# Optimization experiments

Hardware: AMD Instinct MI355X
Metric: run time of the kernel (lower is better)

Reference implementation:

```python
import jax, jax.numpy as jnp
import numpy as np

S, B, H, N, D = 1024, 4, 1024, 16, 64  # seq, batch, d_model, heads, head_dim
P = 2 * S  # relative position length (klen + qlen, no memory)


def rel_shift(x, klen):
    # x: [q, p, b, n] -> shift so position j aligns relatively, keep klen cols
    q, p, b, n = x.shape
    x = jnp.reshape(x, (p, q, b, n))[1:]
    x = jnp.reshape(x, (q, p - 1, b, n))[:, :klen]
    return x


def setup_inputs():
    key = jax.random.key(0)
    ks = jax.random.split(key, 12)
    f32 = jnp.float32
    attention_input = jax.random.normal(ks[0], (S, B, H), f32)
    pos_emb = jax.random.normal(ks[1], (P, B, H), f32)
    seg_embed = jax.random.normal(ks[2], (2, N, D), f32) * 0.02
    # segment matrix: one-hot of whether tokens i,j are in different segments
    seg_ids = jax.random.randint(ks[3], (S, B), 0, 2)
    diff = (seg_ids[:, None, :] != seg_ids[None, :, :]).astype(jnp.int32)
    seg_mat = jax.nn.one_hot(diff, 2, dtype=f32)  # [S,S,B,2]
    r_w_bias = jax.random.normal(ks[4], (N, D), f32) * 0.02
    r_r_bias = jax.random.normal(ks[5], (N, D), f32) * 0.02
    r_s_bias = jax.random.normal(ks[6], (N, D), f32) * 0.02
    # causal mask: 1 where attention is disallowed (j > i)
    causal = jnp.triu(jnp.ones((S, S), f32), k=1)
    attn_mask = jnp.broadcast_to(causal[:, :, None, None], (S, S, B, 1))
    w = lambda k: jax.random.normal(k, (H, N, D), f32) * 0.02
    return {
        'attention_input': attention_input, 'pos_emb': pos_emb,
        'seg_embed': seg_embed, 'seg_mat': seg_mat,
        'r_w_bias': r_w_bias, 'r_r_bias': r_r_bias, 'r_s_bias': r_s_bias,
        'attn_mask': attn_mask,
        'Wq': w(ks[7]), 'Wk': w(ks[8]), 'Wv': w(ks[9]),
        'Wr': w(ks[10]), 'Wo': w(ks[11]),
    }


def reference(attention_input, pos_emb, seg_embed, seg_mat, r_w_bias,
              r_r_bias, r_s_bias, attn_mask, Wq, Wk, Wv, Wr, Wo):
    scale = 1.0 / (D ** 0.5)
    q = jnp.einsum('ibh,hnd->ibnd', attention_input, Wq)
    k = jnp.einsum('ibh,hnd->ibnd', attention_input, Wk)
    v = jnp.einsum('ibh,hnd->ibnd', attention_input, Wv)
    kr = jnp.einsum('ibh,hnd->ibnd', pos_emb, Wr)  # [P,B,N,D]
    # content-based score
    ac = jnp.einsum('ibnd,jbnd->ijbn', q + r_w_bias, k)
    # position-based score with relative shift
    bd = jnp.einsum('ibnd,jbnd->ijbn', q + r_r_bias, kr)
    bd = rel_shift(bd, ac.shape[1])
    # segment-based score
    ef = jnp.einsum('ibnd,snd->ibns', q + r_s_bias, seg_embed)
    ef = jnp.einsum('ijbs,ibns->ijbn', seg_mat, ef)
    attn_score = (ac + bd + ef) * scale - 1e30 * attn_mask
    attn_prob = jax.nn.softmax(attn_score, axis=1)
    attn_vec = jnp.einsum('ijbn,jbnd->ibnd', attn_prob, v)
    attn_out = jnp.einsum('ibnd,hnd->ibh', attn_vec, Wo)
    return attn_out
```

## Files before the change

kernel.cpp:

```cpp
#include <hip/hip_runtime.h>
#include <hip/hip_bf16.h>
#include <stdint.h>


typedef short short8 __attribute__((ext_vector_type(8)));
typedef __bf16 bf16x8 __attribute__((ext_vector_type(8)));
typedef float f32x4 __attribute__((ext_vector_type(4)));
typedef unsigned short u16;
typedef unsigned long long u64;

#define LOG2E 1.4426950408889634f

__device__ __forceinline__ u16 f2bf(float f) {
  union { float f; unsigned u; } v; v.f = f;
  unsigned u = v.u;
  u += 0x7fffu + ((u >> 16) & 1u);
  return (u16)(u >> 16);
}
__device__ __forceinline__ float bf2f(u16 h) {
  union { unsigned u; float f; } v; v.u = ((unsigned)h) << 16;
  return v.f;
}
__device__ __forceinline__ unsigned cvt_pk(float lo, float hi) {
  unsigned r;
  asm("v_cvt_pk_bf16_f32 %0, %1, %2" : "=v"(r) : "v"(lo), "v"(hi));
  return r;
}

__device__ __forceinline__ f32x4 MFMA(short8 a, short8 b, f32x4 c) {
  union { short8 s; bf16x8 v; } ua, ub;
  ua.s = a; ub.s = b;
  return __builtin_amdgcn_mfma_f32_16x16x32_bf16(ua.v, ub.v, c, 0, 0, 0);
}

__device__ __forceinline__ void gload16(const void* g, void* l) {
  __builtin_amdgcn_global_load_lds(
      (const __attribute__((address_space(1))) unsigned int*)g,
      (__attribute__((address_space(3))) unsigned int*)l, 16, 0, 0);
}

__global__ void k_prep(const float* __restrict__ pos, const float* __restrict__ X,
                       const float* __restrict__ Wo, const float* __restrict__ Wq,
                       const float* __restrict__ Wk, const float* __restrict__ Wv,
                       const float* __restrict__ Wr, const float* __restrict__ seg,
                       u16* __restrict__ Pb, u16* __restrict__ Xb, u16* __restrict__ Wob,
                       u16* __restrict__ WT3, u16* __restrict__ WrT, u64* __restrict__ dpw) {
  int bid = blockIdx.x;
  int tid = threadIdx.x;
  if (bid < 9221) {
    const float* in; u16* out; int n, base;
    if (bid < 4101)      { in = pos; out = Pb;  n = 4198400; base = bid; }
    else if (bid < 8197) { in = X;   out = Xb;  n = 4194304; base = bid - 4101; }
    else                 { in = Wo;  out = Wob; n = 1048576; base = bid - 8197; }
    int i = (base * 256 + tid) * 4;
    if (i >= n) return;
    float4 f = *reinterpret_cast<const float4*>(in + i);
    ushort4 o;
    o.x = f2bf(f.x); o.y = f2bf(f.y); o.z = f2bf(f.z); o.w = f2bf(f.w);
    *reinterpret_cast<ushort4*>(out + i) = o;
  } else if (bid < 13317) {
    __shared__ float tile[32][33];
    int tb = bid - 9221;
    int which = tb >> 10;
    int by = (tb >> 5) & 31, bx = tb & 31;
    const float* src = (which == 0) ? Wq : (which == 1) ? Wk : (which == 2) ? Wv : Wr;
    u16* dst = (which < 3) ? (WT3 + (size_t)which * 1048576) : WrT;
    int c0 = bx * 32, h0 = by * 32;
    int tx = tid & 31, ty = tid >> 5;
    for (int r = 0; r < 32; r += 8)
      tile[ty + r][tx] = src[(size_t)(h0 + ty + r) * 1024 + c0 + tx];
    __syncthreads();
    for (int r = 0; r < 32; r += 8)
      dst[(size_t)(c0 + ty + r) * 1024 + h0 + tx] = f2bf(tile[tx][ty + r]);
  } else {
    int W = (bid - 13317) * 4 + (tid >> 6);
    int lane = tid & 63;
    int jt = W & 15, i = W >> 4;
    const float4* p = reinterpret_cast<const float4*>(
        seg + ((size_t)((i << 10) + (jt << 6) + lane)) * 8);
    float4 a = p[0], bq = p[1];
    u64 m0 = __ballot(a.y != 0.f);
    u64 m1 = __ballot(a.w != 0.f);
    u64 m2 = __ballot(bq.y != 0.f);
    u64 m3 = __ballot(bq.w != 0.f);
    if (lane == 0) {
      int o = (i << 4) + jt;
      dpw[o] = m0;
      dpw[16384 + o] = m1;
      dpw[32768 + o] = m2;
      dpw[49152 + o] = m3;
    }
  }
}

__global__ void k_mid(const u16* __restrict__ V, u16* __restrict__ VT,
                      const u16* __restrict__ Q, const float* __restrict__ rsb,
                      const float* __restrict__ segE, float* __restrict__ ef) {
  int bid = blockIdx.x;
  int tid = threadIdx.x;
  if (bid < 1024) {
    __shared__ u16 t[64][68];
    int i0 = (bid & 15) * 64;
    int bn = bid >> 4;
    int tx = tid & 63, ty = tid >> 6;
#pragma unroll
    for (int q = 0; q < 16; q++) {
      int il = ty * 16 + q;
      t[il][tx] = V[(size_t)((bn << 10) + i0 + il) * 64 + tx];
    }
    __syncthreads();
#pragma unroll
    for (int q = 0; q < 16; q++) {
      int d = ty * 16 + q;
      VT[(((size_t)((bn << 6) | d)) << 10) + i0 + tx] = t[tx][d];
    }
  } else {
    int idx = (bid - 1024) * 256 + tid;
    int n = (idx >> 10) & 15;
    float s0 = 0.f, s1 = 0.f;
    const short8* qrow = reinterpret_cast<const short8*>(Q + ((size_t)idx) * 64);
#pragma unroll
    for (int c = 0; c < 8; c++) {
      short8 v = qrow[c];
#pragma unroll
      for (int e = 0; e < 8; e++) {
        int d = c * 8 + e;
        float qv = bf2f((u16)v[e]) + rsb[n * 64 + d];
        s0 += qv * segE[n * 64 + d];
        s1 += qv * segE[1024 + n * 64 + d];
      }
    }
    ef[idx] = (s1 - s0) * (0.125f * LOG2E);
  }
}

__device__ __forceinline__ int srcA_g(int mode, int row, int kk) {
  if (mode == 0) return row * 1024 + kk;
  if (mode == 1) return ((1024 - (row >> 2)) * 4 + (row & 3)) * 1024 + kk;
  int i = row >> 2, b = row & 3, n = kk >> 6, d = kk & 63;
  return (((b << 4) | n) * 1024 + i) * 64 + d;
}

template <int FUSED01>
__global__ __launch_bounds__(256, 2) void k_gemm(const u16* __restrict__ A0,
                                                 const u16* __restrict__ L0,
                                                 const u16* __restrict__ A1,
                                                 const u16* __restrict__ L1,
                                                 void* __restrict__ out0,
                                                 u16* __restrict__ outK,
                                                 u16* __restrict__ outV,
                                                 u16* __restrict__ outR) {
  __shared__ u16 At[128 * 32];
  __shared__ u16 Lt[128 * 32];
  int mode, n0;
  const u16 *A, *L;
  if (FUSED01) {
    if (blockIdx.y < 24) { mode = 0; n0 = blockIdx.y * 128; A = A0; L = L0; }
    else                 { mode = 1; n0 = (blockIdx.y - 24) * 128; A = A1; L = L1; }
  } else {
    mode = 2; n0 = blockIdx.y * 128; A = A0; L = L0;
  }
  int m0 = blockIdx.x * 128;
  int tid = threadIdx.x;
  int w = tid >> 6, lane = tid & 63;
  int lr = lane & 15, lg = lane >> 4;
  int wr = w >> 1, wc = w & 1;
  f32x4 acc[4][4] = {};

  for (int k0 = 0; k0 < 1024; k0 += 32) {
    for (int cc = 0; cc < 2; cc++) {
      int slot = cc * 256 + w * 64 + lane;
      int row = slot >> 2, ch = slot & 3;
      int sch = ch ^ ((row >> 1) & 3);
      gload16(A + srcA_g(mode, m0 + row, k0 + sch * 8), &At[(cc * 256 + w * 64) * 8]);
      gload16(L + (size_t)(n0 + row) * 1024 + k0 + sch * 8, &Lt[(cc * 256 + w * 64) * 8]);
    }
    __syncthreads();
    short8 af[4], bfr[4];
    for (int mt = 0; mt < 4; mt++) {
      int rr = wr * 64 + mt * 16 + lr;
      af[mt] = *reinterpret_cast<const short8*>(&At[rr * 32 + ((lg ^ ((rr >> 1) & 3)) * 8)]);
    }
    for (int ct = 0; ct < 4; ct++) {
      int rr = wc * 64 + ct * 16 + lr;
      bfr[ct] = *reinterpret_cast<const short8*>(&Lt[rr * 32 + ((lg ^ ((rr >> 1) & 3)) * 8)]);
    }
    for (int mt = 0; mt < 4; mt++)
      for (int ct = 0; ct < 4; ct++)
        acc[mt][ct] = MFMA(af[mt], bfr[ct], acc[mt][ct]);
    __syncthreads();
  }

  for (int mt = 0; mt < 4; mt++)
    for (int ct = 0; ct < 4; ct++)
      for (int r = 0; r < 4; r++) {
        int row = m0 + wr * 64 + mt * 16 + lg * 4 + r;
        int col = n0 + wc * 64 + ct * 16 + lr;
        float v = acc[mt][ct][r];
        if (FUSED01 && mode == 0) {
          int i = row >> 2, b = row & 3;
          int which = col >> 10, nd = col & 1023, n = nd >> 6, d = nd & 63;
          u16 hv = f2bf(v);
          int bn = (b << 4) | n;
          if (which == 0)       ((u16*)out0)[(size_t)(bn * 1024 + i) * 64 + d] = hv;
          else if (which == 1)  outK[(size_t)(bn * 1024 + i) * 64 + d] = hv;
          else                  outV[(size_t)(bn * 1024 + i) * 64 + d] = hv;
        } else if (FUSED01) {
          int dist = row >> 2, b = row & 3, n = col >> 6, d = col & 63;
          outR[(size_t)((((b << 4) | n) * 1024 + dist)) * 64 + d] = f2bf(v);
        } else {
          ((float*)out0)[(size_t)row * 1024 + col] = v;
        }
      }
}

__global__ __launch_bounds__(256, 2) void k_attn3(
    const u16* __restrict__ Q, const u16* __restrict__ K, const u16* __restrict__ VT,
    const u16* __restrict__ R, const float* __restrict__ ef,
    const u64* __restrict__ dpw, const float* __restrict__ rwb,
    const float* __restrict__ rrb, float* __restrict__ lsb, u16* __restrict__ pO,
    u16* __restrict__ AV) {
  __shared__ u16 sK[2][64][64];
  __shared__ u16 sV[2][64][64];
  __shared__ u16 sR[2][128][64];
  __shared__ u16 p_lds[4][16][64];
  int f = blockIdx.x + 40 * blockIdx.y;
  int wg = (f & 7) * 320 + (f >> 3);
  int bn = wg / 40;
  int cid = 39 - (wg - bn * 40);
  int b = bn >> 4, n = bn & 15;
  int g = (cid < 4) ? 0 : (cid < 12) ? 1 : (cid < 24) ? 2 : 3;
  int off = cid - 2 * g * (g + 1);
  int qt = 4 * g + off / (g + 1);
  int jc = off % (g + 1);
  int ntiles = (jc < g) ? 4 : (qt + 1 - 4 * g);
  int jt0 = jc * 4;
  int tid = threadIdx.x;
  int w = tid >> 6, lane = tid & 63;
  int lr = lane & 15, lg = lane >> 4;
  int qbase = qt * 64 + w * 16;
  int sub = lane >> 3, ch = lane & 7;
  int cs = (ch ^ sub) * 8;
  int r8 = lr & 7;

  auto stage = [&](int bi, int j0) {
    int rbase = qt * 64 - j0 - 63;
#pragma unroll
    for (int q = 0; q < 2; q++) {
      int row = w * 16 + q * 8 + sub;
      gload16(K + (size_t)((bn << 10) + j0 + row) * 64 + cs, &sK[bi][w * 16 + q * 8][0]);
      gload16(VT + (((size_t)((bn << 6) + row)) << 10) + j0 + cs, &sV[bi][w * 16 + q * 8][0]);
    }
#pragma unroll
    for (int q = 0; q < 4; q++) {
      int pr = w * 32 + q * 8 + sub;
      int ridx = rbase + pr;
      ridx = ridx < 0 ? 0 : (ridx > 1023 ? 1023 : ridx);
      gload16(R + (size_t)((bn << 10) + ridx) * 64 + cs, &sR[bi][w * 32 + q * 8][0]);
    }
  };

  stage(0, jt0 * 64);

  const u64* dwbase = dpw + ((size_t)((b << 10) + qbase + lg * 4) << 4);
  u64 dwc[4], dwn[4] = {0, 0, 0, 0};
#pragma unroll
  for (int r = 0; r < 4; r++) dwc[r] = dwbase[(r << 4) + jt0];

  const float QS = 0.125f * LOG2E;
  short8 qw[2], qr[2];
  for (int ks = 0; ks < 2; ks++) {
    short8 qv = *reinterpret_cast<const short8*>(
        &Q[(size_t)((bn << 10) + qbase + lr) * 64 + ks * 32 + lg * 8]);
    short8 aa, bb;
    for (int e = 0; e < 8; e++) {
      int d = ks * 32 + lg * 8 + e;
      float fq = bf2f((u16)qv[e]);
      aa[e] = (short)f2bf((fq + rwb[n * 64 + d]) * QS);
      bb[e] = (short)f2bf((fq + rrb[n * 64 + d]) * QS);
    }
    qw[ks] = aa;
    qr[ks] = bb;
  }
  short8 ones;
#pragma unroll
  for (int e = 0; e < 8; e++) ones[e] = (short)0x3F80;
  float de[4];
  for (int r = 0; r < 4; r++)
    de[r] = ef[(bn << 10) + qbase + lg * 4 + r];
  float lsum[4] = {0.f, 0.f, 0.f, 0.f};
  f32x4 Oacc[4] = {};

  for (int t = 0; t < ntiles; t++) {
    int jt = jt0 + t;
    int j0 = jt * 64;
    int bi = t & 1;
    asm volatile("s_waitcnt vmcnt(0)" ::: "memory");
    __syncthreads();
    if (t + 1 < ntiles) {
      stage(bi ^ 1, j0 + 64);
#pragma unroll
      for (int r = 0; r < 4; r++) dwn[r] = dwbase[(r << 4) + jt + 1];
    }

    f32x4 sacc[4] = {};
    f32x4 tacc[5] = {};
    __builtin_amdgcn_s_setprio(1);
#pragma unroll
    for (int ks = 0; ks < 2; ks++) {
#pragma unroll
      for (int ct = 0; ct < 4; ct++) {
        short8 kb = *reinterpret_cast<const short8*>(
            &sK[bi][ct * 16 + lr][((ks * 4 + lg) ^ r8) * 8]);
        sacc[ct] = MFMA(qw[ks], kb, sacc[ct]);
      }
#pragma unroll
      for (int ct = 0; ct < 5; ct++) {
        short8 rb = *reinterpret_cast<const short8*>(
            &sR[bi][w * 16 + ct * 16 + lr][((ks * 4 + lg) ^ r8) * 8]);
        tacc[ct] = MFMA(qr[ks], rb, tacc[ct]);
      }
    }
    __builtin_amdgcn_s_setprio(0);

    bool diag = (jt == qt);
#pragma unroll
    for (int r = 0; r < 4; r++) {
      int ii = lg * 4 + r;
      int C0 = 63 + ii - lr;
      int sl = (lg << 4) | (C0 & 15);
      bool hi = (C0 >> 4) == 3;
      float tp0 = __shfl(tacc[0][r], sl);
      float tp1 = __shfl(tacc[1][r], sl);
      float tp2 = __shfl(tacc[2][r], sl);
      float tp3 = __shfl(tacc[3][r], sl);
      float tp4 = __shfl(tacc[4][r], sl);
#pragma unroll
      for (int ct = 0; ct < 4; ct++) {
        float bd;
        if (ct == 0)      bd = hi ? tp3 : tp4;
        else if (ct == 1) bd = hi ? tp2 : tp3;
        else if (ct == 2) bd = hi ? tp1 : tp2;
        else              bd = hi ? tp0 : tp1;
        float s = sacc[ct][r] + bd;
        int jj = ct * 16 + lr;
        if ((dwc[r] >> jj) & 1) s += de[r];
        if (diag && jj > w * 16 + ii) s = -1.0e30f;
        sacc[ct][r] = exp2f(s);
      }
    }
#pragma unroll
    for (int r = 0; r < 4; r++) {
      int ii = lg * 4 + r;
      int sw = (ii & 7) << 3;
      unsigned a01 = cvt_pk(sacc[0][r], sacc[1][r]);
      unsigned a23 = cvt_pk(sacc[2][r], sacc[3][r]);
      p_lds[w][ii][lr ^ sw]        = (u16)a01;
      p_lds[w][ii][(16 + lr) ^ sw] = (u16)(a01 >> 16);
      p_lds[w][ii][(32 + lr) ^ sw] = (u16)a23;
      p_lds[w][ii][(48 + lr) ^ sw] = (u16)(a23 >> 16);
    }
    f32x4 so = {};
    __builtin_amdgcn_s_setprio(1);
#pragma unroll
    for (int ks = 0; ks < 2; ks++) {
      int chunk = ks * 4 + lg;
      short8 afr = *reinterpret_cast<const short8*>(&p_lds[w][lr][(chunk ^ (lr & 7)) * 8]);
      so = MFMA(afr, ones, so);
#pragma unroll
      for (int dt = 0; dt < 4; dt++) {
        short8 vb = *reinterpret_cast<const short8*>(
            &sV[bi][dt * 16 + lr][((ks * 4 + lg) ^ r8) * 8]);
        Oacc[dt] = MFMA(afr, vb, Oacc[dt]);
      }
    }
    __builtin_amdgcn_s_setprio(0);
#pragma unroll
    for (int r = 0; r < 4; r++) lsum[r] += so[r];
#pragma unroll
    for (int r = 0; r < 4; r++) dwc[r] = dwn[r];
  }

  if (g == 0) {
    float inv[4];
#pragma unroll
    for (int r = 0; r < 4; r++) inv[r] = 1.0f / lsum[r];
#pragma unroll
    for (int dt = 0; dt < 4; dt++)
#pragma unroll
      for (int r = 0; r < 4; r++) {
        int qi = qbase + lg * 4 + r;
        AV[(size_t)((bn << 10) + qi) * 64 + dt * 16 + lr] = f2bf(Oacc[dt][r] * inv[r]);
      }
  } else {
    int pid = bn * 40 + cid;
    if (lr == 0)
#pragma unroll
      for (int r = 0; r < 4; r++) {
        int row = w * 16 + lg * 4 + r;
        lsb[(size_t)pid * 64 + row] = lsum[r];
      }
#pragma unroll
    for (int dt = 0; dt < 4; dt++)
#pragma unroll
      for (int r = 0; r < 4; r++) {
        int row = w * 16 + lg * 4 + r;
        pO[(size_t)pid * 4096 + row * 64 + dt * 16 + lr] = f2bf(Oacc[dt][r]);
      }
  }
}

__global__ void k_comb(const float* __restrict__ lsb, const u16* __restrict__ pO,
                       u16* __restrict__ AV) {
  __shared__ float sinv[64];
  int qt = blockIdx.x + 4, bn = blockIdx.y;
  int g = qt >> 2, nc = g + 1;
  int cbase = 2 * g * (g + 1) + (qt - 4 * g) * (g + 1);
  int pid0 = bn * 40 + cbase;
  int t = threadIdx.x;
  if (t < 64) {
    float L = 0.f;
    for (int c2 = 0; c2 < 4; c2++)
      if (c2 < nc) L += lsb[(size_t)(pid0 + c2) * 64 + t];
    sinv[t] = 1.0f / L;
  }
  __syncthreads();
  int dg = t & 7, rowg = t >> 3;
  for (int half = 0; half < 2; half++) {
    int ii = half * 32 + rowg;
    float o[8] = {0, 0, 0, 0, 0, 0, 0, 0};
    for (int c2 = 0; c2 < 4; c2++) {
      if (c2 >= nc) break;
      short8 pv = *reinterpret_cast<const short8*>(
          &pO[(size_t)(pid0 + c2) * 4096 + ii * 64 + dg * 8]);
      for (int e2 = 0; e2 < 8; e2++) o[e2] += bf2f((u16)pv[e2]);
    }
    float s = sinv[ii];
    short8 ov;
    for (int e2 = 0; e2 < 8; e2++) ov[e2] = (short)f2bf(o[e2] * s);
    *reinterpret_cast<short8*>(&AV[(size_t)((bn << 10) + qt * 64 + ii) * 64 + dg * 8]) = ov;
  }
}


extern "C" void kernel_launch(void* const* d_in, const int* in_sizes, int n_in,
                              void* d_out, int out_size, void* d_ws, size_t ws_size,
                              hipStream_t stream) {
  const float* X    = (const float*)d_in[0];
  const float* pos  = (const float*)d_in[1];
  const float* segE = (const float*)d_in[2];
  const float* segM = (const float*)d_in[3];
  const float* rwb  = (const float*)d_in[4];
  const float* rrb  = (const float*)d_in[5];
  const float* rsb  = (const float*)d_in[6];
  const float* Wq = (const float*)d_in[8];
  const float* Wk = (const float*)d_in[9];
  const float* Wv = (const float*)d_in[10];
  const float* Wr = (const float*)d_in[11];
  const float* Wo = (const float*)d_in[12];

  char* ws = (char*)d_ws;
  u16* Xb   = (u16*)(ws);
  u16* Pb   = (u16*)(ws + (8L << 20));
  u16* WT3  = (u16*)(ws + (24L << 20));
  u16* WrT  = (u16*)(ws + (30L << 20));
  u16* Wob  = (u16*)(ws + (32L << 20));
  u16* Qb   = (u16*)(ws + (34L << 20));
  u16* Kb   = (u16*)(ws + (42L << 20));
  u16* VTb  = (u16*)(ws + (50L << 20));
  u16* Rb   = (u16*)(ws + (58L << 20));
  float* efb = (float*)(ws + (66L << 20));
  u64* dpwb = (u64*)(ws + (66L << 20) + (512L << 10));
  float* lsbb = (float*)(ws + (67L << 20));
  u16* pOb  = (u16*)(ws + (69L << 20));
  u16* AVb  = Xb;
  u16* Vtmp = pOb;

  k_prep<<<17413, 256, 0, stream>>>(pos, X, Wo, Wq, Wk, Wv, Wr, segM,
                                    Pb, Xb, Wob, WT3, WrT, dpwb);
  k_gemm<1><<<dim3(32, 32), 256, 0, stream>>>(Xb, WT3, Pb, WrT, Qb, Kb, Vtmp, Rb);
  k_mid<<<1280, 256, 0, stream>>>(Vtmp, VTb, Qb, rsb, segE, efb);
  k_attn3<<<dim3(40, 64), 256, 0, stream>>>(Qb, Kb, VTb, Rb, efb, dpwb, rwb, rrb,
                                            lsbb, pOb, AVb);
  k_comb<<<dim3(12, 64), 256, 0, stream>>>(lsbb, pOb, AVb);
  k_gemm<0><<<dim3(32, 8), 256, 0, stream>>>(AVb, Wob, nullptr, nullptr,
                                             d_out, nullptr, nullptr, nullptr);
}
```

Measured before the change: 164.2 us.

## Load relative-position R fragments directly into registers instead of LDS

Removes the shared-memory staging buffer for the positional key tile R. Each wave now loads its own 80-row band of R straight from global memory into registers (10 short8 fragments), prefetching the next tile's fragments into the same registers after the current tile's positional MFMAs consume them. This removes LDS traffic and frees 32KB of LDS. In exchange it adds 80 VGPRs per lane and duplicates global reads across waves, since the bands overlap instead of sharing one staged tile.

```diff
diff --git a/kernel.cpp b/kernel.cpp
--- a/kernel.cpp
+++ b/kernel.cpp
@@ -222,7 +222,6 @@
     u16* __restrict__ AV) {
   __shared__ u16 sK[2][64][64];
   __shared__ u16 sV[2][64][64];
-  __shared__ u16 sR[2][128][64];
   __shared__ u16 p_lds[4][16][64];
   int f = blockIdx.x + 40 * blockIdx.y;
   int wg = (f & 7) * 320 + (f >> 3);
@@ -244,23 +243,30 @@
   int r8 = lr & 7;
 
   auto stage = [&](int bi, int j0) {
-    int rbase = qt * 64 - j0 - 63;
 #pragma unroll
     for (int q = 0; q < 2; q++) {
       int row = w * 16 + q * 8 + sub;
       gload16(K + (size_t)((bn << 10) + j0 + row) * 64 + cs, &sK[bi][w * 16 + q * 8][0]);
       gload16(VT + (((size_t)((bn << 6) + row)) << 10) + j0 + cs, &sV[bi][w * 16 + q * 8][0]);
     }
-#pragma unroll
-    for (int q = 0; q < 4; q++) {
-      int pr = w * 32 + q * 8 + sub;
-      int ridx = rbase + pr;
-      ridx = ridx < 0 ? 0 : (ridx > 1023 ? 1023 : ridx);
-      gload16(R + (size_t)((bn << 10) + ridx) * 64 + cs, &sR[bi][w * 32 + q * 8][0]);
-    }
   };
 
+  short8 rn[10];
+  auto loadR = [&](int j0) {
+    int band_lo = qbase - j0 - 63;
+#pragma unroll
+    for (int ks = 0; ks < 2; ks++)
+#pragma unroll
+      for (int ct = 0; ct < 5; ct++) {
+        int ridx = band_lo + ct * 16 + lr;
+        ridx = ridx < 0 ? 0 : (ridx > 1023 ? 1023 : ridx);
+        rn[ks * 5 + ct] = *reinterpret_cast<const short8*>(
+            &R[(size_t)((bn << 10) + ridx) * 64 + ks * 32 + lg * 8]);
+      }
+  };
+
   stage(0, jt0 * 64);
+  loadR(jt0 * 64);
 
   const u64* dwbase = dpw + ((size_t)((b << 10) + qbase + lg * 4) << 4);
   u64 dwc[4], dwn[4] = {0, 0, 0, 0};
@@ -297,30 +303,33 @@
     int bi = t & 1;
     asm volatile("s_waitcnt vmcnt(0)" ::: "memory");
     __syncthreads();
+
+    f32x4 tacc[5] = {};
+    __builtin_amdgcn_s_setprio(1);
+#pragma unroll
+    for (int ks = 0; ks < 2; ks++)
+#pragma unroll
+      for (int ct = 0; ct < 5; ct++)
+        tacc[ct] = MFMA(qr[ks], rn[ks * 5 + ct], tacc[ct]);
+    __builtin_amdgcn_s_setprio(0);
+
     if (t + 1 < ntiles) {
       stage(bi ^ 1, j0 + 64);
+      loadR(j0 + 64);
 #pragma unroll
       for (int r = 0; r < 4; r++) dwn[r] = dwbase[(r << 4) + jt + 1];
     }
 
     f32x4 sacc[4] = {};
-    f32x4 tacc[5] = {};
     __builtin_amdgcn_s_setprio(1);
 #pragma unroll
-    for (int ks = 0; ks < 2; ks++) {
+    for (int ks = 0; ks < 2; ks++)
 #pragma unroll
       for (int ct = 0; ct < 4; ct++) {
         short8 kb = *reinterpret_cast<const short8*>(
             &sK[bi][ct * 16 + lr][((ks * 4 + lg) ^ r8) * 8]);
         sacc[ct] = MFMA(qw[ks], kb, sacc[ct]);
       }
-#pragma unroll
-      for (int ct = 0; ct < 5; ct++) {
-        short8 rb = *reinterpret_cast<const short8*>(
-            &sR[bi][w * 16 + ct * 16 + lr][((ks * 4 + lg) ^ r8) * 8]);
-        tacc[ct] = MFMA(qr[ks], rb, tacc[ct]);
-      }
-    }
     __builtin_amdgcn_s_setprio(0);
 
     bool diag = (jt == qt);
```

Result: slower. 184.8 us (+12.6%).
